# Kernel tuning notes

Hardware: AMD Instinct MI355X
Metric: run time of the kernel (lower is better)

Reference implementation:

```python
import jax, jax.numpy as jnp
import numpy as np

N_OBS, N_DIM, N_FUNCTIONS, N_APPLICATIONS = 65536, 256, 16, 8


def setup_inputs() -> dict:
    key = jax.random.key(0)
    k1, k2, k3, k4 = jax.random.split(key, 4)
    x = jax.random.normal(k1, (N_OBS, N_DIM), dtype=jnp.float32)
    function_indices = jax.random.randint(k2, (N_OBS, N_APPLICATIONS), 0, N_FUNCTIONS, dtype=jnp.int32)
    # Stacked Dense weights/biases, one per IFS function. Scale keeps column
    # norms well under the MaxNorm(0.99) constraint (contractive maps).
    W = jax.random.normal(k3, (N_FUNCTIONS, N_DIM, N_DIM), dtype=jnp.float32) * 0.05
    b = jax.random.normal(k4, (N_FUNCTIONS, N_DIM), dtype=jnp.float32) * 0.05
    return {"x": x, "function_indices": function_indices, "W": W, "b": b}


def reference(x, function_indices, W, b):
    # One IFS application step: compute all n_functions affine maps for every
    # point (as the original layer does), then select the per-point function.
    def step(carry, idx):
        # carry: (n_obs, n_dim); idx: (n_obs,) int
        y_all = jnp.einsum('od,fde->ofe', carry, W) + b  # (n_obs, n_funcs, n_dim)
        y = jnp.take_along_axis(y_all, idx[:, None, None].astype(jnp.int32), axis=1)[:, 0, :]
        return y, None
    # scan over the n_applications axis (leading axis after transpose)
    out, _ = jax.lax.scan(step, x, function_indices.T)
    return out
```

## Files before the change

kernel.cpp:

```cpp
#include <hip/hip_runtime.h>
#include <hip/hip_bf16.h>
#include <stdint.h>

#define N_OBS 65536
#define N_DIM 256
#define N_FUN 16
#define N_APP 8
#define MT 64
#define PERM_STRIDE (N_OBS + N_FUN * MT)
#define MAX_TILES (PERM_STRIDE / MT)
#define N_BLK 256

typedef __attribute__((ext_vector_type(8))) short v8s;
typedef __attribute__((ext_vector_type(4))) float v4f;

__device__ __forceinline__ unsigned short f2bf(float f) {
  union { float f; uint32_t u; } v;
  v.f = f;
  uint32_t u = v.u;
  return (unsigned short)((u + 0x7FFFu + ((u >> 16) & 1u)) >> 16);
}

__global__ void k_init(int* __restrict__ perm) {
  int tid = blockIdx.x * 256 + threadIdx.x;
  if (tid < N_APP * PERM_STRIDE) perm[tid] = -1;
}

__global__ void k_prep_w(const float* __restrict__ W, unsigned short* __restrict__ Wt) {
  int tid = blockIdx.x * 256 + threadIdx.x;
  int f = tid >> 16;
  int n = (tid >> 8) & 255;
  int k = tid & 255;
  Wt[tid] = f2bf(W[(f << 16) | (k << 8) | n]);
}

__global__ void k_hist2(const int* __restrict__ fidx, int* __restrict__ blockCnt) {
  __shared__ int h[N_APP * N_FUN];
  int tid = threadIdx.x;
  if (tid < N_APP * N_FUN) h[tid] = 0;
  __syncthreads();
  int o = blockIdx.x * 256 + tid;
  const int4* p = (const int4*)(fidx + o * N_APP);
  int4 a = p[0], b = p[1];
  atomicAdd(&h[0 * N_FUN + a.x], 1);
  atomicAdd(&h[1 * N_FUN + a.y], 1);
  atomicAdd(&h[2 * N_FUN + a.z], 1);
  atomicAdd(&h[3 * N_FUN + a.w], 1);
  atomicAdd(&h[4 * N_FUN + b.x], 1);
  atomicAdd(&h[5 * N_FUN + b.y], 1);
  atomicAdd(&h[6 * N_FUN + b.z], 1);
  atomicAdd(&h[7 * N_FUN + b.w], 1);
  __syncthreads();
  if (tid < N_APP * N_FUN) blockCnt[tid * N_BLK + blockIdx.x] = h[tid];
}

__global__ void k_scan2(const int* __restrict__ blockCnt, int* __restrict__ pb,
                        int* __restrict__ tilef, int* __restrict__ blockOff) {
  __shared__ int tot[N_APP * N_FUN];
  int i = threadIdx.x;
  if (i < N_APP * N_FUN) {
    int s = 0;
    for (int b = 0; b < N_BLK; ++b) s += blockCnt[i * N_BLK + b];
    tot[i] = s;
  }
  __syncthreads();
  if (i < N_APP) {
    int base = 0;
    for (int f = 0; f < N_FUN; ++f) {
      pb[i * 17 + f] = base;
      int c = tot[i * N_FUN + f];
      int padded = (c + MT - 1) & ~(MT - 1);
      int q0 = base / MT, q1 = (base + padded) / MT;
      for (int q = q0; q < q1; ++q) tilef[i * MAX_TILES + q] = f;
      base += padded;
    }
    pb[i * 17 + 16] = base;
  }
  __syncthreads();
  if (i < N_APP * N_FUN) {
    int t = i >> 4, f = i & 15;
    int off = pb[t * 17 + f];
    for (int b = 0; b < N_BLK; ++b) {
      blockOff[i * N_BLK + b] = off;
      off += blockCnt[i * N_BLK + b];
    }
  }
}

__global__ void k_scatter2(const int* __restrict__ fidx, const int* __restrict__ blockOff,
                           int* __restrict__ perm) {
  __shared__ int cur[N_APP * N_FUN];
  int tid = threadIdx.x;
  if (tid < N_APP * N_FUN) cur[tid] = blockOff[tid * N_BLK + blockIdx.x];
  __syncthreads();
  int o = blockIdx.x * 256 + tid;
  const int4* p = (const int4*)(fidx + o * N_APP);
  int4 a = p[0], b = p[1];
  int fs[8] = {a.x, a.y, a.z, a.w, b.x, b.y, b.z, b.w};
  #pragma unroll
  for (int t = 0; t < N_APP; ++t) {
    int pos = atomicAdd(&cur[t * N_FUN + fs[t]], 1);
    perm[t * PERM_STRIDE + pos] = o;
  }
}

template <bool SRC_F32, bool DST_F32>
__global__ __launch_bounds__(256, 2)
void k_step(const void* __restrict__ src_, void* __restrict__ dst_,
            const unsigned short* __restrict__ Wt, const float* __restrict__ bias,
            const int* __restrict__ perm_t, const int* __restrict__ pb_t,
            const int* __restrict__ tilef_t) {
  __shared__ unsigned short As[MT * N_DIM];
  int tile = blockIdx.x;
  if (tile * MT >= pb_t[16]) return;
  int f = tilef_t[tile];
  int tid = threadIdx.x;
  const int* permBase = perm_t + tile * MT;

  #pragma unroll
  for (int i = 0; i < 8; ++i) {
    int chunk = tid + i * 256;
    int row = chunk >> 5;
    int c = chunk & 31;
    int grow = permBase[row];
    unsigned short* d =
        (unsigned short*)((char*)As + (row << 9) + ((c << 4) ^ ((row & 7) << 4)));
    v8s val = {0, 0, 0, 0, 0, 0, 0, 0};
    if (grow >= 0) {
      if (SRC_F32) {
        const v4f* s = (const v4f*)((const float*)src_ + ((size_t)grow << 8) + (c << 3));
        v4f v0 = s[0], v1 = s[1];
        val[0] = (short)f2bf(v0[0]);
        val[1] = (short)f2bf(v0[1]);
        val[2] = (short)f2bf(v0[2]);
        val[3] = (short)f2bf(v0[3]);
        val[4] = (short)f2bf(v1[0]);
        val[5] = (short)f2bf(v1[1]);
        val[6] = (short)f2bf(v1[2]);
        val[7] = (short)f2bf(v1[3]);
      } else {
        val = *(const v8s*)((const unsigned short*)src_ + ((size_t)grow << 8) + (c << 3));
      }
    }
    *(v8s*)d = val;
  }
  __syncthreads();

  int lane = tid & 63;
  int wave = tid >> 6;
  int l15 = lane & 15;
  int lq = lane >> 4;

  v4f acc[4][4] = {};
  const unsigned short* Wf = Wt + (size_t)f * N_DIM * N_DIM;

  #pragma unroll
  for (int kk = 0; kk < 8; ++kk) {
    v8s a[4];
    #pragma unroll
    for (int mt = 0; mt < 4; ++mt) {
      int row = mt * 16 + l15;
      int byte = (row << 9) + ((((kk << 2) + lq) << 4) ^ ((row & 7) << 4));
      a[mt] = *(const v8s*)((const char*)As + byte);
    }
    #pragma unroll
    for (int nt = 0; nt < 4; ++nt) {
      int n = wave * 64 + nt * 16 + l15;
      v8s bfr = *(const v8s*)(Wf + n * N_DIM + (kk << 5) + (lq << 3));
      #pragma unroll
      for (int mt = 0; mt < 4; ++mt)
        acc[mt][nt] = __builtin_amdgcn_mfma_f32_16x16x32_bf16(a[mt], bfr, acc[mt][nt], 0, 0, 0);
    }
  }

  int grows[4][4];
  #pragma unroll
  for (int mt = 0; mt < 4; ++mt)
    #pragma unroll
    for (int r = 0; r < 4; ++r)
      grows[mt][r] = permBase[mt * 16 + lq * 4 + r];

  const float* bf_ = bias + f * N_DIM;
  #pragma unroll
  for (int nt = 0; nt < 4; ++nt) {
    int n = wave * 64 + nt * 16 + l15;
    float bv = bf_[n];
    #pragma unroll
    for (int mt = 0; mt < 4; ++mt) {
      #pragma unroll
      for (int r = 0; r < 4; ++r) {
        int grow = grows[mt][r];
        if (grow >= 0) {
          float v = acc[mt][nt][r] + bv;
          if (DST_F32)
            ((float*)dst_)[((size_t)grow << 8) + n] = v;
          else
            ((unsigned short*)dst_)[((size_t)grow << 8) + n] = f2bf(v);
        }
      }
    }
  }
}

extern "C" void kernel_launch(void* const* d_in, const int* in_sizes, int n_in,
                              void* d_out, int out_size, void* d_ws, size_t ws_size,
                              hipStream_t stream) {
  const float* x = (const float*)d_in[0];
  const int* fidx = (const int*)d_in[1];
  const float* W = (const float*)d_in[2];
  const float* bias = (const float*)d_in[3];

  char* ws = (char*)d_ws;
  unsigned short* carryA = (unsigned short*)ws;
  int* blockCnt = (int*)ws;
  int* blockOff = (int*)(ws + 131072);
  unsigned short* Wt = (unsigned short*)(ws + (size_t)33554432);
  int* perm   = (int*)(ws + 35651584);
  int* pb     = (int*)(ws + 37781504);
  int* tilef  = (int*)(ws + 37782048);
  unsigned short* carryB = (unsigned short*)d_out;

  k_init<<<(N_APP * PERM_STRIDE + 255) / 256, 256, 0, stream>>>(perm);
  k_prep_w<<<(N_FUN * N_DIM * N_DIM) / 256, 256, 0, stream>>>(W, Wt);
  k_hist2<<<N_BLK, 256, 0, stream>>>(fidx, blockCnt);
  k_scan2<<<1, 128, 0, stream>>>(blockCnt, pb, tilef, blockOff);
  k_scatter2<<<N_BLK, 256, 0, stream>>>(fidx, blockOff, perm);

  k_step<true, false><<<MAX_TILES, 256, 0, stream>>>(x, carryA, Wt, bias, perm, pb, tilef);
  for (int t = 1; t < 7; ++t) {
    const unsigned short* s = (t & 1) ? carryA : carryB;
    unsigned short* d = (t & 1) ? carryB : carryA;
    k_step<false, false><<<MAX_TILES, 256, 0, stream>>>(
        s, d, Wt, bias, perm + t * PERM_STRIDE, pb + t * 17, tilef + t * MAX_TILES);
  }
  k_step<false, true><<<MAX_TILES, 256, 0, stream>>>(
      carryA, d_out, Wt, bias, perm + 7 * PERM_STRIDE, pb + 7 * 17, tilef + 7 * MAX_TILES);
}
```

Before: 443.3 us.

## Store intermediate carries in next step's permuted order to make loads contiguous

Precomputes, for each step, the slot each point occupies in the next step's sorted permutation, then writes the bf16 carry directly into that permuted position. Each subsequent step can then read its tile as a contiguous block instead of gathering rows. Outputs are staged through shared memory for row-wise vector stores, and the MFMA operands are swapped so the final fp32 store writes four contiguous floats. It adds two small index-building kernels and raises the occupancy hint to 4.

```diff
diff --git a/kernel.cpp b/kernel.cpp
--- a/kernel.cpp
+++ b/kernel.cpp
@@ -12,6 +12,7 @@
 #define N_BLK 256
 
 typedef __attribute__((ext_vector_type(8))) short v8s;
+typedef __attribute__((ext_vector_type(4))) short v4s;
 typedef __attribute__((ext_vector_type(4))) float v4f;
 
 __device__ __forceinline__ unsigned short f2bf(float f) {
@@ -104,55 +105,75 @@
   }
 }
 
-template <bool SRC_F32, bool DST_F32>
-__global__ __launch_bounds__(256, 2)
+__global__ void k_pos(const int* __restrict__ perm, int* __restrict__ pos) {
+  int tid = blockIdx.x * 256 + threadIdx.x;
+  if (tid >= 7 * PERM_STRIDE) return;
+  int t = tid / PERM_STRIDE + 1;
+  int s = tid - (t - 1) * PERM_STRIDE;
+  int o = perm[t * PERM_STRIDE + s];
+  if (o >= 0) pos[(t - 1) * N_OBS + o] = s;
+}
+
+__global__ void k_outpos(int* __restrict__ perm, const int* __restrict__ pos,
+                         int* __restrict__ outpos0) {
+  int tid = blockIdx.x * 256 + threadIdx.x;
+  if (tid >= 7 * PERM_STRIDE) return;
+  int t = tid / PERM_STRIDE;
+  int s = tid - t * PERM_STRIDE;
+  int o = perm[t * PERM_STRIDE + s];
+  int val = (o >= 0) ? pos[t * N_OBS + o] : -1;
+  if (t == 0) outpos0[s] = val;
+  else perm[t * PERM_STRIDE + s] = val;
+}
+
+template <int SRC_F32, int DST_F32>
+__global__ __launch_bounds__(256, 4)
 void k_step(const void* __restrict__ src_, void* __restrict__ dst_,
             const unsigned short* __restrict__ Wt, const float* __restrict__ bias,
-            const int* __restrict__ perm_t, const int* __restrict__ pb_t,
-            const int* __restrict__ tilef_t) {
+            const int* __restrict__ pb_t, const int* __restrict__ tilef_t,
+            const int* __restrict__ outpos_t, const int* __restrict__ perm0) {
   __shared__ unsigned short As[MT * N_DIM];
+  __shared__ int ops[MT];
   int tile = blockIdx.x;
   if (tile * MT >= pb_t[16]) return;
   int f = tilef_t[tile];
   int tid = threadIdx.x;
-  const int* permBase = perm_t + tile * MT;
-
-  #pragma unroll
-  for (int i = 0; i < 8; ++i) {
-    int chunk = tid + i * 256;
-    int row = chunk >> 5;
-    int c = chunk & 31;
-    int grow = permBase[row];
-    unsigned short* d =
-        (unsigned short*)((char*)As + (row << 9) + ((c << 4) ^ ((row & 7) << 4)));
-    v8s val = {0, 0, 0, 0, 0, 0, 0, 0};
-    if (grow >= 0) {
-      if (SRC_F32) {
-        const v4f* s = (const v4f*)((const float*)src_ + ((size_t)grow << 8) + (c << 3));
-        v4f v0 = s[0], v1 = s[1];
-        val[0] = (short)f2bf(v0[0]);
-        val[1] = (short)f2bf(v0[1]);
-        val[2] = (short)f2bf(v0[2]);
-        val[3] = (short)f2bf(v0[3]);
-        val[4] = (short)f2bf(v1[0]);
-        val[5] = (short)f2bf(v1[1]);
-        val[6] = (short)f2bf(v1[2]);
-        val[7] = (short)f2bf(v1[3]);
-      } else {
-        val = *(const v8s*)((const unsigned short*)src_ + ((size_t)grow << 8) + (c << 3));
-      }
-    }
-    *(v8s*)d = val;
-  }
-  __syncthreads();
-
-  int lane = tid & 63;
-  int wave = tid >> 6;
-  int l15 = lane & 15;
-  int lq = lane >> 4;
-
+
+  if (tid < MT) ops[tid] = outpos_t[tile * MT + tid];
+
+  if (SRC_F32) {
+    const int* permBase = perm0 + tile * MT;
+    #pragma unroll
+    for (int i = 0; i < 8; ++i) {
+      int g = tid + i * 256;
+      int row = g >> 5, c = g & 31;
+      int grow = permBase[row];
+      if (grow < 0) grow = 0;
+      const v4f* s = (const v4f*)((const float*)src_ + ((size_t)grow << 8) + (c << 3));
+      v4f v0 = s[0], v1 = s[1];
+      v8s val;
+      val[0] = (short)f2bf(v0[0]); val[1] = (short)f2bf(v0[1]);
+      val[2] = (short)f2bf(v0[2]); val[3] = (short)f2bf(v0[3]);
+      val[4] = (short)f2bf(v1[0]); val[5] = (short)f2bf(v1[1]);
+      val[6] = (short)f2bf(v1[2]); val[7] = (short)f2bf(v1[3]);
+      *(v8s*)((char*)As + (row << 9) + ((c ^ (row & 7)) << 4)) = val;
+    }
+  } else {
+    const unsigned short* srcT = (const unsigned short*)src_ + (size_t)tile * MT * N_DIM;
+    #pragma unroll
+    for (int i = 0; i < 8; ++i) {
+      int g = tid + i * 256;
+      int row = g >> 5, c = g & 31;
+      v8s val = *(const v8s*)(srcT + (size_t)g * 8);
+      *(v8s*)((char*)As + (row << 9) + ((c ^ (row & 7)) << 4)) = val;
+    }
+  }
+  __syncthreads();
+
+  int lane = tid & 63, wave = tid >> 6;
+  int l15 = lane & 15, lq = lane >> 4;
   v4f acc[4][4] = {};
-  const unsigned short* Wf = Wt + (size_t)f * N_DIM * N_DIM;
+  const unsigned short* Wf = Wt + ((size_t)f << 16);
 
   #pragma unroll
   for (int kk = 0; kk < 8; ++kk) {
@@ -160,7 +181,7 @@
     #pragma unroll
     for (int mt = 0; mt < 4; ++mt) {
       int row = mt * 16 + l15;
-      int byte = (row << 9) + ((((kk << 2) + lq) << 4) ^ ((row & 7) << 4));
+      int byte = (row << 9) + ((((kk << 2) + lq) ^ (row & 7)) << 4);
       a[mt] = *(const v8s*)((const char*)As + byte);
     }
     #pragma unroll
@@ -169,34 +190,55 @@
       v8s bfr = *(const v8s*)(Wf + n * N_DIM + (kk << 5) + (lq << 3));
       #pragma unroll
       for (int mt = 0; mt < 4; ++mt)
-        acc[mt][nt] = __builtin_amdgcn_mfma_f32_16x16x32_bf16(a[mt], bfr, acc[mt][nt], 0, 0, 0);
-    }
-  }
-
-  int grows[4][4];
-  #pragma unroll
-  for (int mt = 0; mt < 4; ++mt)
-    #pragma unroll
-    for (int r = 0; r < 4; ++r)
-      grows[mt][r] = permBase[mt * 16 + lq * 4 + r];
+        acc[mt][nt] = __builtin_amdgcn_mfma_f32_16x16x32_bf16(bfr, a[mt], acc[mt][nt], 0, 0, 0);
+    }
+  }
 
   const float* bf_ = bias + f * N_DIM;
-  #pragma unroll
-  for (int nt = 0; nt < 4; ++nt) {
-    int n = wave * 64 + nt * 16 + l15;
-    float bv = bf_[n];
+  if (DST_F32) {
+    float* dout = (float*)dst_;
     #pragma unroll
     for (int mt = 0; mt < 4; ++mt) {
+      int m = mt * 16 + l15;
+      int orow = ops[m];
+      if (orow >= 0) {
+        #pragma unroll
+        for (int nt = 0; nt < 4; ++nt) {
+          int n0 = wave * 64 + nt * 16 + lq * 4;
+          v4f bv = *(const v4f*)(bf_ + n0);
+          v4f o = acc[mt][nt] + bv;
+          *(v4f*)(dout + ((size_t)orow << 8) + n0) = o;
+        }
+      }
+    }
+  } else {
+    __syncthreads();
+    #pragma unroll
+    for (int mt = 0; mt < 4; ++mt) {
+      int m = mt * 16 + l15;
       #pragma unroll
-      for (int r = 0; r < 4; ++r) {
-        int grow = grows[mt][r];
-        if (grow >= 0) {
-          float v = acc[mt][nt][r] + bv;
-          if (DST_F32)
-            ((float*)dst_)[((size_t)grow << 8) + n] = v;
-          else
-            ((unsigned short*)dst_)[((size_t)grow << 8) + n] = f2bf(v);
-        }
+      for (int nt = 0; nt < 4; ++nt) {
+        int n0 = wave * 64 + nt * 16 + lq * 4;
+        v4f bv = *(const v4f*)(bf_ + n0);
+        v4s pk;
+        pk[0] = (short)f2bf(acc[mt][nt][0] + bv[0]);
+        pk[1] = (short)f2bf(acc[mt][nt][1] + bv[1]);
+        pk[2] = (short)f2bf(acc[mt][nt][2] + bv[2]);
+        pk[3] = (short)f2bf(acc[mt][nt][3] + bv[3]);
+        int c = n0 >> 3;
+        *(v4s*)((char*)As + (m << 9) + ((c ^ (m & 7)) << 4) + ((n0 & 7) << 1)) = pk;
+      }
+    }
+    __syncthreads();
+    unsigned short* dst = (unsigned short*)dst_;
+    #pragma unroll
+    for (int i = 0; i < 8; ++i) {
+      int g = tid + i * 256;
+      int row = g >> 5, c = g & 31;
+      int op = ops[row];
+      if (op >= 0) {
+        v8s v = *(const v8s*)((char*)As + (row << 9) + ((c ^ (row & 7)) << 4));
+        *(v8s*)(dst + (size_t)op * N_DIM + c * 8) = v;
       }
     }
   }
@@ -214,10 +256,12 @@
   unsigned short* carryA = (unsigned short*)ws;
   int* blockCnt = (int*)ws;
   int* blockOff = (int*)(ws + 131072);
-  unsigned short* Wt = (unsigned short*)(ws + (size_t)33554432);
-  int* perm   = (int*)(ws + 35651584);
-  int* pb     = (int*)(ws + 37781504);
-  int* tilef  = (int*)(ws + 37782048);
+  int* pos      = (int*)(ws + 262144);
+  unsigned short* Wt = (unsigned short*)(ws + 34078720);
+  int* perm    = (int*)(ws + 36175872);
+  int* pb      = (int*)(ws + 38305792);
+  int* tilef   = (int*)(ws + 38306336);
+  int* outpos0 = (int*)(ws + 38339648);
   unsigned short* carryB = (unsigned short*)d_out;
 
   k_init<<<(N_APP * PERM_STRIDE + 255) / 256, 256, 0, stream>>>(perm);
@@ -225,14 +269,18 @@
   k_hist2<<<N_BLK, 256, 0, stream>>>(fidx, blockCnt);
   k_scan2<<<1, 128, 0, stream>>>(blockCnt, pb, tilef, blockOff);
   k_scatter2<<<N_BLK, 256, 0, stream>>>(fidx, blockOff, perm);
-
-  k_step<true, false><<<MAX_TILES, 256, 0, stream>>>(x, carryA, Wt, bias, perm, pb, tilef);
+  k_pos<<<(7 * PERM_STRIDE + 255) / 256, 256, 0, stream>>>(perm, pos);
+  k_outpos<<<(7 * PERM_STRIDE + 255) / 256, 256, 0, stream>>>(perm, pos, outpos0);
+
+  k_step<1, 0><<<MAX_TILES, 256, 0, stream>>>(x, carryA, Wt, bias, pb, tilef, outpos0, perm);
   for (int t = 1; t < 7; ++t) {
     const unsigned short* s = (t & 1) ? carryA : carryB;
     unsigned short* d = (t & 1) ? carryB : carryA;
-    k_step<false, false><<<MAX_TILES, 256, 0, stream>>>(
-        s, d, Wt, bias, perm + t * PERM_STRIDE, pb + t * 17, tilef + t * MAX_TILES);
-  }
-  k_step<false, true><<<MAX_TILES, 256, 0, stream>>>(
-      carryA, d_out, Wt, bias, perm + 7 * PERM_STRIDE, pb + 7 * 17, tilef + 7 * MAX_TILES);
-}
+    k_step<0, 0><<<MAX_TILES, 256, 0, stream>>>(
+        s, d, Wt, bias, pb + t * 17, tilef + t * MAX_TILES,
+        perm + t * PERM_STRIDE, nullptr);
+  }
+  k_step<0, 1><<<MAX_TILES, 256, 0, stream>>>(
+      carryA, d_out, Wt, bias, pb + 7 * 17, tilef + 7 * MAX_TILES,
+      perm + 7 * PERM_STRIDE, nullptr);
+}
```

New measurement: 388.1 us. 12.5% less time.
